# Kernel optimization log

Hardware: AMD Instinct MI355X
Metric: run time of the kernel (lower is better)

The kernel has to match this reference:

```python
import jax, jax.numpy as jnp
import numpy as np

N, E, D_IN, D_HID, D_OUT = 50000, 800000, 64, 128, 64


def setup_inputs() -> dict:
    key = jax.random.key(0)
    ks = jax.random.split(key, 8)
    x = jax.random.normal(ks[0], (N, D_IN), dtype=jnp.float32)
    edge_index = jax.random.randint(ks[1], (2, E), 0, N, dtype=jnp.int64)
    # SAGEConv layer 1: lin_l (agg path, with bias), lin_r (root path, no bias)
    s1 = 1.0 / np.sqrt(D_IN)
    W_l1 = jax.random.uniform(ks[2], (D_HID, D_IN), jnp.float32, -s1, s1)
    b_l1 = jnp.zeros((D_HID,), jnp.float32)
    W_r1 = jax.random.uniform(ks[3], (D_HID, D_IN), jnp.float32, -s1, s1)
    s2 = 1.0 / np.sqrt(D_HID)
    W_l2 = jax.random.uniform(ks[4], (D_OUT, D_HID), jnp.float32, -s2, s2)
    b_l2 = jnp.zeros((D_OUT,), jnp.float32)
    W_r2 = jax.random.uniform(ks[5], (D_OUT, D_HID), jnp.float32, -s2, s2)
    return {"x": x, "edge_index": edge_index,
            "W_l1": W_l1, "b_l1": b_l1, "W_r1": W_r1,
            "W_l2": W_l2, "b_l2": b_l2, "W_r2": W_r2}


def _sage_layer(h, src, dst, W_l, b_l, W_r, n_nodes):
    # scatter-mean of source features onto targets
    msg = h[src]                                               # [E, d]
    summed = jax.ops.segment_sum(msg, dst, num_segments=n_nodes)
    deg = jax.ops.segment_sum(jnp.ones((src.shape[0], 1), h.dtype), dst,
                              num_segments=n_nodes)
    agg = summed / jnp.maximum(deg, 1.0)                       # [n, d]
    return agg @ W_l.T + b_l + h @ W_r.T


def reference(x, edge_index, W_l1, b_l1, W_r1, W_l2, b_l2, W_r2):
    src, dst = edge_index[0], edge_index[1]
    n = x.shape[0]
    h = _sage_layer(x, src, dst, W_l1, b_l1, W_r1, n)
    h = jnp.tanh(h)
    h = _sage_layer(h, src, dst, W_l2, b_l2, W_r2, n)
    return jax.nn.log_softmax(h, axis=1)
```

## Files before the change

kernel.cpp:

```cpp
#include <hip/hip_runtime.h>
#include <hip/hip_bf16.h>
#include <math.h>


typedef unsigned short u16;
typedef unsigned int   u32;
typedef __attribute__((ext_vector_type(8))) __bf16 bf16x8;
typedef __attribute__((ext_vector_type(4))) float  f32x4;

__device__ __forceinline__ u16 f2bf(float f) {
    u32 u = __float_as_uint(f);
    u32 r = (u + 0x7FFFu + ((u >> 16) & 1u)) >> 16;
    return (u16)r;
}
__device__ __forceinline__ float bfl(u32 u) { return __uint_as_float(u << 16); }
__device__ __forceinline__ float bfh(u32 u) { return __uint_as_float(u & 0xFFFF0000u); }
__device__ __forceinline__ u32 pack2(float a, float b) {
    return (u32)f2bf(a) | ((u32)f2bf(b) << 16);
}
__device__ __forceinline__ int pad16(int x) { return (x + 15) & ~15; }

__global__ __launch_bounds__(256) void misc_kernel(
    const float* __restrict__ x, uint4* __restrict__ xb4, int nCvt8,
    const float* __restrict__ Wl1, const float* __restrict__ Wr1,
    const float* __restrict__ Wl2, const float* __restrict__ Wr2,
    u16* __restrict__ W1c, u16* __restrict__ W2c,
    u16* __restrict__ perm, int permStore8,
    int* __restrict__ cnt, int nCnt4,
    u16* __restrict__ xb, u16* __restrict__ m2b,
    int N, int VB, int PB, int ZB)
{
    int blk = blockIdx.x, tid = threadIdx.x;
    if (blk < VB) {
        int i = blk * 256 + tid;
        if (i < nCvt8) {
            float4 v0 = ((const float4*)x)[i * 2];
            float4 v1 = ((const float4*)x)[i * 2 + 1];
            uint4 p;
            p.x = pack2(v0.x, v0.y); p.y = pack2(v0.z, v0.w);
            p.z = pack2(v1.x, v1.y); p.w = pack2(v1.z, v1.w);
            xb4[i] = p;
        }
    } else if (blk < VB + 64) {
        int i = (blk - VB) * 256 + tid;
        if (i < 128 * 128) {
            int o = i >> 7, k = i & 127;
            float w1 = (k < 64) ? Wr1[o * 64 + k] : Wl1[o * 64 + (k - 64)];
            W1c[i] = f2bf(w1);
            float w2 = (o < 64) ? Wl2[o * 128 + k] : Wr2[(o - 64) * 128 + k];
            W2c[i] = f2bf(w2);
        }
    } else if (blk < VB + 64 + PB) {
        int i = (blk - VB - 64) * 256 + tid;
        if (i < permStore8) {
            u32 v = (u32)N | ((u32)N << 16);
            uint4 q; q.x = v; q.y = v; q.z = v; q.w = v;
            ((uint4*)perm)[i] = q;
        }
    } else if (blk < VB + 64 + PB + ZB) {
        int i = (blk - VB - 64 - PB) * 256 + tid;
        if (i < nCnt4) {
            uint4 z; z.x = 0; z.y = 0; z.z = 0; z.w = 0;
            ((uint4*)cnt)[i] = z;
        }
    } else {
        if (tid < 32)      ((u32*)(xb  + (size_t)N * 64))[tid] = 0;
        else if (tid < 64) ((u32*)(m2b + (size_t)N * 64))[tid - 32] = 0;
    }
}

__global__ __launch_bounds__(256) void fill_kernel(
    const int* __restrict__ src, const int* __restrict__ dst,
    int* __restrict__ cnt, u16* __restrict__ perm, int E, int N8, float invN8)
{
    int g = blockIdx.x & 7;
    int e0 = (blockIdx.x >> 3) * 2048 + threadIdx.x * 8;
    int d[8];
    if (e0 + 8 <= E) {
        int4 d0 = *(const int4*)(dst + e0);
        int4 d1 = *(const int4*)(dst + e0 + 4);
        d[0] = d0.x; d[1] = d0.y; d[2] = d0.z; d[3] = d0.w;
        d[4] = d1.x; d[5] = d1.y; d[6] = d1.z; d[7] = d1.w;
    } else {
        for (int k = 0; k < 8; k++) d[k] = (e0 + k < E) ? dst[e0 + k] : -1;
    }
#pragma unroll
    for (int k = 0; k < 8; k++) {
        int dd = d[k];
        if (dd < 0) continue;
        int b = (int)((float)dd * invN8);
        if (dd >= (b + 1) * N8) b++;
        else if (dd < b * N8) b--;
        if (b != g) continue;
        int pos = atomicAdd(&cnt[dd], 1);
        if (pos < 64) perm[(size_t)dd * 64 + pos] = (u16)src[e0 + k];
    }
}

__device__ __forceinline__ void gather_core(
    const u32* __restrict__ feat2, const u16* __restrict__ perm,
    int lo, int hi, int lane, int quarter, int c, float acc[4])
{
    float a0 = 0.f, a1 = 0.f, a2 = 0.f, a3 = 0.f;
    float b0 = 0.f, b1 = 0.f, b2 = 0.f, b3 = 0.f;
    float c0 = 0.f, c1 = 0.f, c2 = 0.f, c3 = 0.f;
    float d0 = 0.f, d1 = 0.f, d2 = 0.f, d3 = 0.f;
    for (int base = lo; base < hi; base += 64) {
        int pidx = (int)perm[base + lane];
        int rem = min(64, hi - base);
        for (int j = 0; j < rem; j += 16) {
            int r0 = __shfl(pidx, j + quarter,      64);
            int r1 = __shfl(pidx, j + 4 + quarter,  64);
            int r2 = __shfl(pidx, j + 8 + quarter,  64);
            int r3 = __shfl(pidx, j + 12 + quarter, 64);
            uint2 u0 = *(const uint2*)(feat2 + (size_t)r0 * 32 + c * 2);
            uint2 u1 = *(const uint2*)(feat2 + (size_t)r1 * 32 + c * 2);
            uint2 u2 = *(const uint2*)(feat2 + (size_t)r2 * 32 + c * 2);
            uint2 u3 = *(const uint2*)(feat2 + (size_t)r3 * 32 + c * 2);
            a0 += bfl(u0.x); a1 += bfh(u0.x); a2 += bfl(u0.y); a3 += bfh(u0.y);
            b0 += bfl(u1.x); b1 += bfh(u1.x); b2 += bfl(u1.y); b3 += bfh(u1.y);
            c0 += bfl(u2.x); c1 += bfh(u2.x); c2 += bfl(u2.y); c3 += bfh(u2.y);
            d0 += bfl(u3.x); d1 += bfh(u3.x); d2 += bfl(u3.y); d3 += bfh(u3.y);
        }
    }
    acc[0] = (a0 + b0) + (c0 + d0);
    acc[1] = (a1 + b1) + (c1 + d1);
    acc[2] = (a2 + b2) + (c2 + d2);
    acc[3] = (a3 + b3) + (c3 + d3);
}

__global__ __launch_bounds__(256) void gather1_kernel(
    const u32* __restrict__ xb2, const u16* __restrict__ perm,
    const int* __restrict__ cnt, u32* __restrict__ aggb2, int N)
{
    int wid  = blockIdx.x * 4 + (threadIdx.x >> 6);
    int lane = threadIdx.x & 63;
    if (wid >= N) return;
    int deg = cnt[wid];
    int lo = wid * 64;
    int hi = lo + pad16(min(deg, 64));
    int quarter = lane >> 4, c = lane & 15;
    float acc[4];
    gather_core(xb2, perm, lo, hi, lane, quarter, c, acc);
#pragma unroll
    for (int i = 0; i < 4; i++) {
        acc[i] += __shfl_xor(acc[i], 16, 64);
        acc[i] += __shfl_xor(acc[i], 32, 64);
    }
    if (quarter == 0) {
        float inv = 1.f / fmaxf((float)deg, 1.f);
        uint2 p;
        p.x = pack2(acc[0] * inv, acc[1] * inv);
        p.y = pack2(acc[2] * inv, acc[3] * inv);
        *(uint2*)(aggb2 + (size_t)wid * 32 + c * 2) = p;
    }
}

__global__ __launch_bounds__(256) void layer12_mfma(
    const u16* __restrict__ xb, const u16* __restrict__ aggb,
    const u16* __restrict__ W1, const float* __restrict__ b1,
    const u16* __restrict__ W2, const float* __restrict__ b2,
    u16* __restrict__ m2b, float* __restrict__ out, int N)
{
    __shared__ u16 tile[4][2048];
    int tid = threadIdx.x;
    int wv = tid >> 6, lane = tid & 63;
    int quad = lane >> 4, l16 = lane & 15;
    int node = blockIdx.x * 64 + wv * 16 + l16;
    int nclamp = min(node, N - 1);
    const u16* xrow = xb   + (size_t)nclamp * 64;
    const u16* arow = aggb + (size_t)nclamp * 64;
    bf16x8 a0 = *(const bf16x8*)(xrow + quad * 8);
    bf16x8 a1 = *(const bf16x8*)(xrow + 32 + quad * 8);
    bf16x8 a2 = *(const bf16x8*)(arow + quad * 8);
    bf16x8 a3 = *(const bf16x8*)(arow + 32 + quad * 8);
#pragma unroll
    for (int nt = 0; nt < 8; nt++) {
        const u16* wrow = W1 + (size_t)(nt * 16 + l16) * 128 + quad * 8;
        f32x4 acc = {0.f, 0.f, 0.f, 0.f};
        acc = __builtin_amdgcn_mfma_f32_16x16x32_bf16(a0, *(const bf16x8*)(wrow),      acc, 0, 0, 0);
        acc = __builtin_amdgcn_mfma_f32_16x16x32_bf16(a1, *(const bf16x8*)(wrow + 32), acc, 0, 0, 0);
        acc = __builtin_amdgcn_mfma_f32_16x16x32_bf16(a2, *(const bf16x8*)(wrow + 64), acc, 0, 0, 0);
        acc = __builtin_amdgcn_mfma_f32_16x16x32_bf16(a3, *(const bf16x8*)(wrow + 96), acc, 0, 0, 0);
        int col = nt * 16 + l16;
        float bias = b1[col];
#pragma unroll
        for (int r = 0; r < 4; r++) {
            int row = quad * 4 + r;
            tile[wv][row * 128 + (col ^ ((row & 7) << 3))] =
                f2bf(tanhf(acc[r] + bias));
        }
    }
    __syncthreads();
    int swz = (l16 & 7) << 3;
    bf16x8 h0 = *(const bf16x8*)&tile[wv][l16 * 128 + (( 0 + quad * 8) ^ swz)];
    bf16x8 h1 = *(const bf16x8*)&tile[wv][l16 * 128 + ((32 + quad * 8) ^ swz)];
    bf16x8 h2 = *(const bf16x8*)&tile[wv][l16 * 128 + ((64 + quad * 8) ^ swz)];
    bf16x8 h3 = *(const bf16x8*)&tile[wv][l16 * 128 + ((96 + quad * 8) ^ swz)];
    int orow = blockIdx.x * 64 + wv * 16 + quad * 4;
#pragma unroll
    for (int nt = 0; nt < 8; nt++) {
        const u16* wrow = W2 + (size_t)(nt * 16 + l16) * 128 + quad * 8;
        f32x4 acc = {0.f, 0.f, 0.f, 0.f};
        acc = __builtin_amdgcn_mfma_f32_16x16x32_bf16(h0, *(const bf16x8*)(wrow),      acc, 0, 0, 0);
        acc = __builtin_amdgcn_mfma_f32_16x16x32_bf16(h1, *(const bf16x8*)(wrow + 32), acc, 0, 0, 0);
        acc = __builtin_amdgcn_mfma_f32_16x16x32_bf16(h2, *(const bf16x8*)(wrow + 64), acc, 0, 0, 0);
        acc = __builtin_amdgcn_mfma_f32_16x16x32_bf16(h3, *(const bf16x8*)(wrow + 96), acc, 0, 0, 0);
        int oc = nt * 16 + l16;
#pragma unroll
        for (int r = 0; r < 4; r++) {
            int nn = orow + r;
            if (nn >= N) continue;
            if (oc < 64) m2b[(size_t)nn * 64 + oc] = f2bf(acc[r]);
            else         out[(size_t)nn * 64 + (oc - 64)] = acc[r] + b2[oc - 64];
        }
    }
}

__global__ __launch_bounds__(256) void gather2_final_kernel(
    const u32* __restrict__ m2b2, const u16* __restrict__ perm,
    const int* __restrict__ cnt, float* __restrict__ out, int N)
{
    int wid  = blockIdx.x * 4 + (threadIdx.x >> 6);
    int lane = threadIdx.x & 63;
    if (wid >= N) return;
    int deg = cnt[wid];
    int lo = wid * 64;
    int hi = lo + pad16(min(deg, 64));
    int quarter = lane >> 4, c = lane & 15;
    float acc[4];
    gather_core(m2b2, perm, lo, hi, lane, quarter, c, acc);
#pragma unroll
    for (int i = 0; i < 4; i++) {
        acc[i] += __shfl_xor(acc[i], 16, 64);
        acc[i] += __shfl_xor(acc[i], 32, 64);
    }
    float inv = 1.f / fmaxf((float)deg, 1.f);
    float4 r2 = ((const float4*)(out + (size_t)wid * 64))[c];
    float v0 = acc[0] * inv + r2.x;
    float v1 = acc[1] * inv + r2.y;
    float v2 = acc[2] * inv + r2.z;
    float v3 = acc[3] * inv + r2.w;
    float m = fmaxf(fmaxf(v0, v1), fmaxf(v2, v3));
#pragma unroll
    for (int o = 1; o < 16; o <<= 1) m = fmaxf(m, __shfl_xor(m, o, 64));
    float sum = expf(v0 - m) + expf(v1 - m) + expf(v2 - m) + expf(v3 - m);
#pragma unroll
    for (int o = 1; o < 16; o <<= 1) sum += __shfl_xor(sum, o, 64);
    if (quarter == 0) {
        float ls = m + logf(sum);
        float4 res = make_float4(v0 - ls, v1 - ls, v2 - ls, v3 - ls);
        ((float4*)(out + (size_t)wid * 64))[c] = res;
    }
}

extern "C" void kernel_launch(void* const* d_in, const int* in_sizes, int n_in,
                              void* d_out, int out_size, void* d_ws, size_t ws_size,
                              hipStream_t stream)
{
    const float* x   = (const float*)d_in[0];
    const int*   ei  = (const int*)d_in[1];
    const float* Wl1 = (const float*)d_in[2];
    const float* bl1 = (const float*)d_in[3];
    const float* Wr1 = (const float*)d_in[4];
    const float* Wl2 = (const float*)d_in[5];
    const float* bl2 = (const float*)d_in[6];
    const float* Wr2 = (const float*)d_in[7];
    float* out = (float*)d_out;

    int N = in_sizes[0] / 64;
    int E = in_sizes[1] / 2;
    const int* src = ei;
    const int* dst = ei + E;
    int N8 = (N + 7) / 8;
    float invN8 = 1.0f / (float)N8;

    size_t permN = (size_t)N * 64;
    int permStore8 = (int)(permN / 8);
    int PB = (permStore8 + 255) / 256;

    char* wsb = (char*)d_ws;
    size_t npad = ((size_t)N + 64) & ~(size_t)63;
    int* cnt  = (int*)wsb;
    u16* perm = (u16*)(cnt + npad);
    u16* xb   = perm + permN;
    u16* aggb = xb + (size_t)(N + 1) * 64;
    u16* m2b  = aggb + (size_t)N * 64;
    u16* W1c  = m2b + (size_t)(N + 1) * 64;
    u16* W2c  = W1c + 128 * 128;

    int nCvt8 = N * 64 / 8;
    int VB = (nCvt8 + 255) / 256;
    int nCnt4 = N / 4;
    int ZB = (nCnt4 + 255) / 256;
    misc_kernel<<<VB + 64 + PB + ZB + 1, 256, 0, stream>>>(
        x, (uint4*)xb, nCvt8,
        Wl1, Wr1, Wl2, Wr2, W1c, W2c,
        perm, permStore8, cnt, nCnt4, xb, m2b, N, VB, PB, ZB);

    {
        int chunks = (E + 2047) / 2048;
        fill_kernel<<<chunks * 8, 256, 0, stream>>>(src, dst, cnt, perm, E,
                                                    N8, invN8);
    }

    gather1_kernel<<<(N + 3) / 4, 256, 0, stream>>>((const u32*)xb, perm,
                                                    cnt, (u32*)aggb, N);

    layer12_mfma<<<(N + 63) / 64, 256, 0, stream>>>(xb, aggb, W1c, bl1,
                                                    W2c, bl2, m2b, out, N);

    gather2_final_kernel<<<(N + 3) / 4, 256, 0, stream>>>((const u32*)m2b, perm,
                                                          cnt, out, N);
}
```

Before: 202.4 us.

## Split feature tables into column halves and map each half to separate XCD groups

Feature tables (x, aggregated, and layer-2 messages) are stored as two 32-column halves. The gather kernels run twice as many blocks, and the block-to-XCD mapping sends each half to a distinct group of four XCDs, so each XCD's L2 only has to cache half of the table. The fused gather2 and softmax kernel is split into a half-gather that writes fp32 means to workspace and a separate softmax kernel. This adds an extra launch and extra global traffic for the means, and each gather lane now issues narrower 4-byte loads.

```diff
diff --git a/kernel.cpp b/kernel.cpp
--- a/kernel.cpp
+++ b/kernel.cpp
@@ -21,13 +21,15 @@
 __device__ __forceinline__ int pad16(int x) { return (x + 15) & ~15; }
 
 __global__ __launch_bounds__(256) void misc_kernel(
-    const float* __restrict__ x, uint4* __restrict__ xb4, int nCvt8,
+    const float* __restrict__ x, uint4* __restrict__ xbA4,
+    uint4* __restrict__ xbB4, int nCvt8,
     const float* __restrict__ Wl1, const float* __restrict__ Wr1,
     const float* __restrict__ Wl2, const float* __restrict__ Wr2,
     u16* __restrict__ W1c, u16* __restrict__ W2c,
     u16* __restrict__ perm, int permStore8,
     int* __restrict__ cnt, int nCnt4,
-    u16* __restrict__ xb, u16* __restrict__ m2b,
+    u16* __restrict__ xbA, u16* __restrict__ xbB,
+    u16* __restrict__ m2bA, u16* __restrict__ m2bB,
     int N, int VB, int PB, int ZB)
 {
     int blk = blockIdx.x, tid = threadIdx.x;
@@ -39,7 +41,9 @@
             uint4 p;
             p.x = pack2(v0.x, v0.y); p.y = pack2(v0.z, v0.w);
             p.z = pack2(v1.x, v1.y); p.w = pack2(v1.z, v1.w);
-            xb4[i] = p;
+            int row = i >> 3, cb = i & 7;
+            if (cb < 4) xbA4[row * 4 + cb]       = p;
+            else        xbB4[row * 4 + (cb - 4)] = p;
         }
     } else if (blk < VB + 64) {
         int i = (blk - VB) * 256 + tid;
@@ -64,8 +68,10 @@
             ((uint4*)cnt)[i] = z;
         }
     } else {
-        if (tid < 32)      ((u32*)(xb  + (size_t)N * 64))[tid] = 0;
-        else if (tid < 64) ((u32*)(m2b + (size_t)N * 64))[tid - 32] = 0;
+        if (tid < 16)      ((u32*)(xbA  + (size_t)N * 32))[tid]      = 0;
+        else if (tid < 32) ((u32*)(xbB  + (size_t)N * 32))[tid - 16] = 0;
+        else if (tid < 48) ((u32*)(m2bA + (size_t)N * 32))[tid - 32] = 0;
+        else if (tid < 64) ((u32*)(m2bB + (size_t)N * 32))[tid - 48] = 0;
     }
 }
 
@@ -97,14 +103,12 @@
     }
 }
 
-__device__ __forceinline__ void gather_core(
-    const u32* __restrict__ feat2, const u16* __restrict__ perm,
-    int lo, int hi, int lane, int quarter, int c, float acc[4])
-{
-    float a0 = 0.f, a1 = 0.f, a2 = 0.f, a3 = 0.f;
-    float b0 = 0.f, b1 = 0.f, b2 = 0.f, b3 = 0.f;
-    float c0 = 0.f, c1 = 0.f, c2 = 0.f, c3 = 0.f;
-    float d0 = 0.f, d1 = 0.f, d2 = 0.f, d3 = 0.f;
+__device__ __forceinline__ void gather_half(
+    const u32* __restrict__ tab, const u16* __restrict__ perm,
+    int lo, int hi, int lane, int quarter, int c, float acc[2])
+{
+    float a0 = 0.f, a1 = 0.f, b0 = 0.f, b1 = 0.f;
+    float c0 = 0.f, c1 = 0.f, d0 = 0.f, d1 = 0.f;
     for (int base = lo; base < hi; base += 64) {
         int pidx = (int)perm[base + lane];
         int rem = min(64, hi - base);
@@ -113,54 +117,91 @@
             int r1 = __shfl(pidx, j + 4 + quarter,  64);
             int r2 = __shfl(pidx, j + 8 + quarter,  64);
             int r3 = __shfl(pidx, j + 12 + quarter, 64);
-            uint2 u0 = *(const uint2*)(feat2 + (size_t)r0 * 32 + c * 2);
-            uint2 u1 = *(const uint2*)(feat2 + (size_t)r1 * 32 + c * 2);
-            uint2 u2 = *(const uint2*)(feat2 + (size_t)r2 * 32 + c * 2);
-            uint2 u3 = *(const uint2*)(feat2 + (size_t)r3 * 32 + c * 2);
-            a0 += bfl(u0.x); a1 += bfh(u0.x); a2 += bfl(u0.y); a3 += bfh(u0.y);
-            b0 += bfl(u1.x); b1 += bfh(u1.x); b2 += bfl(u1.y); b3 += bfh(u1.y);
-            c0 += bfl(u2.x); c1 += bfh(u2.x); c2 += bfl(u2.y); c3 += bfh(u2.y);
-            d0 += bfl(u3.x); d1 += bfh(u3.x); d2 += bfl(u3.y); d3 += bfh(u3.y);
+            u32 u0 = tab[(size_t)r0 * 16 + c];
+            u32 u1 = tab[(size_t)r1 * 16 + c];
+            u32 u2 = tab[(size_t)r2 * 16 + c];
+            u32 u3 = tab[(size_t)r3 * 16 + c];
+            a0 += bfl(u0); a1 += bfh(u0);
+            b0 += bfl(u1); b1 += bfh(u1);
+            c0 += bfl(u2); c1 += bfh(u2);
+            d0 += bfl(u3); d1 += bfh(u3);
         }
     }
     acc[0] = (a0 + b0) + (c0 + d0);
     acc[1] = (a1 + b1) + (c1 + d1);
-    acc[2] = (a2 + b2) + (c2 + d2);
-    acc[3] = (a3 + b3) + (c3 + d3);
-}
-
-__global__ __launch_bounds__(256) void gather1_kernel(
-    const u32* __restrict__ xb2, const u16* __restrict__ perm,
-    const int* __restrict__ cnt, u32* __restrict__ aggb2, int N)
-{
-    int wid  = blockIdx.x * 4 + (threadIdx.x >> 6);
+}
+
+__device__ __forceinline__ void split_ids(int bid, int tid, int* half, int* wid)
+{
+    int xcdg = bid & 7;
+    *half = xcdg >> 2;
+    int slot = (bid >> 3) * 4 + (xcdg & 3);
+    *wid = slot * 4 + (tid >> 6);
+}
+
+__global__ __launch_bounds__(256) void gather1_split(
+    const u32* __restrict__ xbA2, const u32* __restrict__ xbB2,
+    const u16* __restrict__ perm, const int* __restrict__ cnt,
+    u32* __restrict__ aggA2, u32* __restrict__ aggB2, int N)
+{
+    int half, wid;
+    split_ids(blockIdx.x, threadIdx.x, &half, &wid);
     int lane = threadIdx.x & 63;
     if (wid >= N) return;
     int deg = cnt[wid];
     int lo = wid * 64;
     int hi = lo + pad16(min(deg, 64));
     int quarter = lane >> 4, c = lane & 15;
-    float acc[4];
-    gather_core(xb2, perm, lo, hi, lane, quarter, c, acc);
-#pragma unroll
-    for (int i = 0; i < 4; i++) {
+    const u32* tab = half ? xbB2 : xbA2;
+    float acc[2];
+    gather_half(tab, perm, lo, hi, lane, quarter, c, acc);
+#pragma unroll
+    for (int i = 0; i < 2; i++) {
         acc[i] += __shfl_xor(acc[i], 16, 64);
         acc[i] += __shfl_xor(acc[i], 32, 64);
     }
     if (quarter == 0) {
         float inv = 1.f / fmaxf((float)deg, 1.f);
-        uint2 p;
-        p.x = pack2(acc[0] * inv, acc[1] * inv);
-        p.y = pack2(acc[2] * inv, acc[3] * inv);
-        *(uint2*)(aggb2 + (size_t)wid * 32 + c * 2) = p;
+        u32* agg = half ? aggB2 : aggA2;
+        agg[(size_t)wid * 16 + c] = pack2(acc[0] * inv, acc[1] * inv);
+    }
+}
+
+__global__ __launch_bounds__(256) void gather2_split(
+    const u32* __restrict__ m2bA2, const u32* __restrict__ m2bB2,
+    const u16* __restrict__ perm, const int* __restrict__ cnt,
+    float2* __restrict__ meanA2, float2* __restrict__ meanB2, int N)
+{
+    int half, wid;
+    split_ids(blockIdx.x, threadIdx.x, &half, &wid);
+    int lane = threadIdx.x & 63;
+    if (wid >= N) return;
+    int deg = cnt[wid];
+    int lo = wid * 64;
+    int hi = lo + pad16(min(deg, 64));
+    int quarter = lane >> 4, c = lane & 15;
+    const u32* tab = half ? m2bB2 : m2bA2;
+    float acc[2];
+    gather_half(tab, perm, lo, hi, lane, quarter, c, acc);
+#pragma unroll
+    for (int i = 0; i < 2; i++) {
+        acc[i] += __shfl_xor(acc[i], 16, 64);
+        acc[i] += __shfl_xor(acc[i], 32, 64);
+    }
+    if (quarter == 0) {
+        float inv = 1.f / fmaxf((float)deg, 1.f);
+        float2* mean = half ? meanB2 : meanA2;
+        mean[(size_t)wid * 16 + c] = make_float2(acc[0] * inv, acc[1] * inv);
     }
 }
 
 __global__ __launch_bounds__(256) void layer12_mfma(
-    const u16* __restrict__ xb, const u16* __restrict__ aggb,
+    const u16* __restrict__ xbA, const u16* __restrict__ xbB,
+    const u16* __restrict__ aggA, const u16* __restrict__ aggB,
     const u16* __restrict__ W1, const float* __restrict__ b1,
     const u16* __restrict__ W2, const float* __restrict__ b2,
-    u16* __restrict__ m2b, float* __restrict__ out, int N)
+    u16* __restrict__ m2bA, u16* __restrict__ m2bB,
+    float* __restrict__ out, int N)
 {
     __shared__ u16 tile[4][2048];
     int tid = threadIdx.x;
@@ -168,12 +209,10 @@
     int quad = lane >> 4, l16 = lane & 15;
     int node = blockIdx.x * 64 + wv * 16 + l16;
     int nclamp = min(node, N - 1);
-    const u16* xrow = xb   + (size_t)nclamp * 64;
-    const u16* arow = aggb + (size_t)nclamp * 64;
-    bf16x8 a0 = *(const bf16x8*)(xrow + quad * 8);
-    bf16x8 a1 = *(const bf16x8*)(xrow + 32 + quad * 8);
-    bf16x8 a2 = *(const bf16x8*)(arow + quad * 8);
-    bf16x8 a3 = *(const bf16x8*)(arow + 32 + quad * 8);
+    bf16x8 a0 = *(const bf16x8*)(xbA  + (size_t)nclamp * 32 + quad * 8);
+    bf16x8 a1 = *(const bf16x8*)(xbB  + (size_t)nclamp * 32 + quad * 8);
+    bf16x8 a2 = *(const bf16x8*)(aggA + (size_t)nclamp * 32 + quad * 8);
+    bf16x8 a3 = *(const bf16x8*)(aggB + (size_t)nclamp * 32 + quad * 8);
 #pragma unroll
     for (int nt = 0; nt < 8; nt++) {
         const u16* wrow = W1 + (size_t)(nt * 16 + l16) * 128 + quad * 8;
@@ -211,47 +250,30 @@
         for (int r = 0; r < 4; r++) {
             int nn = orow + r;
             if (nn >= N) continue;
-            if (oc < 64) m2b[(size_t)nn * 64 + oc] = f2bf(acc[r]);
-            else         out[(size_t)nn * 64 + (oc - 64)] = acc[r] + b2[oc - 64];
-        }
-    }
-}
-
-__global__ __launch_bounds__(256) void gather2_final_kernel(
-    const u32* __restrict__ m2b2, const u16* __restrict__ perm,
-    const int* __restrict__ cnt, float* __restrict__ out, int N)
+            if (oc < 32)      m2bA[(size_t)nn * 32 + oc]        = f2bf(acc[r]);
+            else if (oc < 64) m2bB[(size_t)nn * 32 + (oc - 32)] = f2bf(acc[r]);
+            else out[(size_t)nn * 64 + (oc - 64)] = acc[r] + b2[oc - 64];
+        }
+    }
+}
+
+__global__ __launch_bounds__(256) void final_softmax(
+    const float* __restrict__ meanA, const float* __restrict__ meanB,
+    float* __restrict__ out, int N)
 {
     int wid  = blockIdx.x * 4 + (threadIdx.x >> 6);
     int lane = threadIdx.x & 63;
     if (wid >= N) return;
-    int deg = cnt[wid];
-    int lo = wid * 64;
-    int hi = lo + pad16(min(deg, 64));
-    int quarter = lane >> 4, c = lane & 15;
-    float acc[4];
-    gather_core(m2b2, perm, lo, hi, lane, quarter, c, acc);
-#pragma unroll
-    for (int i = 0; i < 4; i++) {
-        acc[i] += __shfl_xor(acc[i], 16, 64);
-        acc[i] += __shfl_xor(acc[i], 32, 64);
-    }
-    float inv = 1.f / fmaxf((float)deg, 1.f);
-    float4 r2 = ((const float4*)(out + (size_t)wid * 64))[c];
-    float v0 = acc[0] * inv + r2.x;
-    float v1 = acc[1] * inv + r2.y;
-    float v2 = acc[2] * inv + r2.z;
-    float v3 = acc[3] * inv + r2.w;
-    float m = fmaxf(fmaxf(v0, v1), fmaxf(v2, v3));
-#pragma unroll
-    for (int o = 1; o < 16; o <<= 1) m = fmaxf(m, __shfl_xor(m, o, 64));
-    float sum = expf(v0 - m) + expf(v1 - m) + expf(v2 - m) + expf(v3 - m);
-#pragma unroll
-    for (int o = 1; o < 16; o <<= 1) sum += __shfl_xor(sum, o, 64);
-    if (quarter == 0) {
-        float ls = m + logf(sum);
-        float4 res = make_float4(v0 - ls, v1 - ls, v2 - ls, v3 - ls);
-        ((float4*)(out + (size_t)wid * 64))[c] = res;
-    }
+    int h = lane >> 5, c5 = lane & 31;
+    float mv = h ? meanB[(size_t)wid * 32 + c5] : meanA[(size_t)wid * 32 + c5];
+    float v = mv + out[(size_t)wid * 64 + lane];
+    float m = v;
+#pragma unroll
+    for (int o = 1; o < 64; o <<= 1) m = fmaxf(m, __shfl_xor(m, o, 64));
+    float s = expf(v - m);
+#pragma unroll
+    for (int o = 1; o < 64; o <<= 1) s += __shfl_xor(s, o, 64);
+    out[(size_t)wid * 64 + lane] = v - (m + logf(s));
 }
 
 extern "C" void kernel_launch(void* const* d_in, const int* in_sizes, int n_in,
@@ -283,20 +305,25 @@
     size_t npad = ((size_t)N + 64) & ~(size_t)63;
     int* cnt  = (int*)wsb;
     u16* perm = (u16*)(cnt + npad);
-    u16* xb   = perm + permN;
-    u16* aggb = xb + (size_t)(N + 1) * 64;
-    u16* m2b  = aggb + (size_t)N * 64;
-    u16* W1c  = m2b + (size_t)(N + 1) * 64;
+    u16* xbA  = perm + permN;
+    u16* xbB  = xbA + (size_t)(N + 1) * 32;
+    u16* aggA = xbB + (size_t)(N + 1) * 32;
+    u16* aggB = aggA + (size_t)N * 32;
+    u16* m2bA = aggB + (size_t)N * 32;
+    u16* m2bB = m2bA + (size_t)(N + 1) * 32;
+    u16* W1c  = m2bB + (size_t)(N + 1) * 32;
     u16* W2c  = W1c + 128 * 128;
+    float* meanA = (float*)(W2c + 128 * 128);
+    float* meanB = meanA + (size_t)N * 32;
 
     int nCvt8 = N * 64 / 8;
     int VB = (nCvt8 + 255) / 256;
     int nCnt4 = N / 4;
     int ZB = (nCnt4 + 255) / 256;
     misc_kernel<<<VB + 64 + PB + ZB + 1, 256, 0, stream>>>(
-        x, (uint4*)xb, nCvt8,
+        x, (uint4*)xbA, (uint4*)xbB, nCvt8,
         Wl1, Wr1, Wl2, Wr2, W1c, W2c,
-        perm, permStore8, cnt, nCnt4, xb, m2b, N, VB, PB, ZB);
+        perm, permStore8, cnt, nCnt4, xbA, xbB, m2bA, m2bB, N, VB, PB, ZB);
 
     {
         int chunks = (E + 2047) / 2048;
@@ -304,12 +331,18 @@
                                                     N8, invN8);
     }
 
-    gather1_kernel<<<(N + 3) / 4, 256, 0, stream>>>((const u32*)xb, perm,
-                                                    cnt, (u32*)aggb, N);
-
-    layer12_mfma<<<(N + 63) / 64, 256, 0, stream>>>(xb, aggb, W1c, bl1,
-                                                    W2c, bl2, m2b, out, N);
-
-    gather2_final_kernel<<<(N + 3) / 4, 256, 0, stream>>>((const u32*)m2b, perm,
-                                                          cnt, out, N);
-}
+    int gatherGrid = ((N + 3) / 4) * 2;
+
+    gather1_split<<<gatherGrid, 256, 0, stream>>>(
+        (const u32*)xbA, (const u32*)xbB, perm, cnt,
+        (u32*)aggA, (u32*)aggB, N);
+
+    layer12_mfma<<<(N + 63) / 64, 256, 0, stream>>>(
+        xbA, xbB, aggA, aggB, W1c, bl1, W2c, bl2, m2bA, m2bB, out, N);
+
+    gather2_split<<<gatherGrid, 256, 0, stream>>>(
+        (const u32*)m2bA, (const u32*)m2bB, perm, cnt,
+        (float2*)meanA, (float2*)meanB, N);
+
+    final_softmax<<<(N + 3) / 4, 256, 0, stream>>>(meanA, meanB, out, N);
+}
```

Measured after the change: 223.8 us. 1.11x slower.
